# Performance work log

Measured on AMD Instinct MI355X. Metric: run time of the kernel, lower is better.

The kernel has to match this reference:

```python
import jax, jax.numpy as jnp
import numpy as np

IN_CH = 32
OUT_CH = 32
HIDDEN = 32  # edge/angle MLP hidden width


def setup_inputs() -> dict:
    key = jax.random.key(0)
    ks = jax.random.split(key, 13)
    N, E, A = 50000, 200000, 400000
    s = 0.1
    return {
        "x": jax.random.normal(ks[0], (N, IN_CH), dtype=jnp.float32),
        "edge_index": jax.random.randint(ks[1], (2, E), 0, N),
        "edge_attr": jax.random.uniform(ks[2], (E, 1), dtype=jnp.float32),
        "angle_index": jax.random.randint(ks[3], (3, A), 0, N),
        "angles": jax.random.uniform(ks[4], (A, 1), dtype=jnp.float32),
        # edge_mlp: Linear(1,32) -> ReLU -> Linear(32, in*out)
        "eW1": jax.random.normal(ks[5], (1, HIDDEN), dtype=jnp.float32) * s,
        "eb1": jax.random.normal(ks[6], (HIDDEN,), dtype=jnp.float32) * s,
        "eW2": jax.random.normal(ks[7], (HIDDEN, IN_CH * OUT_CH), dtype=jnp.float32) * s,
        "eb2": jax.random.normal(ks[8], (IN_CH * OUT_CH,), dtype=jnp.float32) * s,
        # angle_mlp: Linear(1,32) -> ReLU -> Linear(32, out)
        "aW1": jax.random.normal(ks[9], (1, HIDDEN), dtype=jnp.float32) * s,
        "ab1": jax.random.normal(ks[10], (HIDDEN,), dtype=jnp.float32) * s,
        "aW2": jax.random.normal(ks[11], (HIDDEN, OUT_CH), dtype=jnp.float32) * s,
        "ab2": jax.random.normal(ks[12], (OUT_CH,), dtype=jnp.float32) * s,
    }


def reference(x, edge_index, edge_attr, angle_index, angles,
              eW1, eb1, eW2, eb2, aW1, ab1, aW2, ab2):
    N = x.shape[0]
    row, col = edge_index[0], edge_index[1]
    # per-edge weight matrices from edge MLP: (E, in, out)
    h = jax.nn.relu(edge_attr @ eW1 + eb1)
    edge_w = (h @ eW2 + eb2).reshape(-1, IN_CH, OUT_CH)
    # gather source node features, apply per-edge matrix (bmm)
    msg = jnp.einsum('ei,eio->eo', x[col], edge_w)  # (E, out)
    agg = jax.ops.segment_sum(msg, row, num_segments=N)
    # angle branch: scatter angle features onto center node j
    j = angle_index[1]
    angle_feat = jax.nn.relu(angles @ aW1 + ab1) @ aW2 + ab2  # (A, out)
    agg = agg + jax.ops.segment_sum(angle_feat, j, num_segments=N)
    return agg
```

## Files before the change

kernel.cpp:

```cpp
#include <hip/hip_runtime.h>
#include <hip/hip_bf16.h>
#include <stdint.h>

#define IC 32
#define OC 32
#define HID 32

#define PBIN 16
#define TSH 44
#define TSCALE 1048576.0f

#define PBE 12
#define MAXN 65536

typedef __attribute__((ext_vector_type(8))) _Float16 half8;
typedef __attribute__((ext_vector_type(4))) float f32x4;
typedef unsigned long long u64;

static __device__ __forceinline__ _Float16 f2h(float f) { return (_Float16)f; }

__device__ __align__(16) _Float16 g_MK[PBE * 2 * 32 * 32];
__device__ float g_ekn[16];
__device__ float g_akn[16];
__device__ int   g_npc[2];
__device__ __align__(16) u64 g_cells[(size_t)MAXN * PBIN];

__global__ __launch_bounds__(512) void setup_zero(
    const float* __restrict__ eW1, const float* __restrict__ eb1,
    const float* __restrict__ eW2, const float* __restrict__ eb2,
    const float* __restrict__ aW1, const float* __restrict__ ab1,
    float* __restrict__ out, int outF4, int cellF4)
{
    __shared__ float ts_s[32];
    __shared__ int   rk_s[32];
    __shared__ int   re_s[32];
    const int tid = threadIdx.x;
    const int bid = blockIdx.x;

    if (bid < 48) {
        if (bid == 0 && tid < 16) { g_ekn[tid] = 1e30f; g_akn[tid] = 1e30f; }
        if (tid < 32) {
            const int k = tid;
            const float w = eW1[k], b = eb1[k];
            const float ts = -b / w;
            const bool re = (w != 0.f) && (ts > 0.f) && (ts < 1.f);
            int rk = 0;
            for (int k2 = 0; k2 < 32; ++k2) {
                const float w2 = eW1[k2], b2 = eb1[k2];
                const float t2 = -b2 / w2;
                const bool re2 = (w2 != 0.f) && (t2 > 0.f) && (t2 < 1.f);
                rk += (re2 && (t2 < ts || (t2 == ts && k2 < k))) ? 1 : 0;
            }
            ts_s[k] = ts; rk_s[k] = rk; re_s[k] = re ? 1 : 0;
        }
        __syncthreads();

        if (bid == 0) {
            if (tid < 32) {
                if (re_s[tid]) g_ekn[rk_s[tid]] = ts_s[tid];
                if (tid == 0) {
                    int n = 0;
                    for (int k = 0; k < 32; ++k) n += re_s[k];
                    g_npc[0] = n + 1;
                }
            } else if (tid < 64) {
                const int k = tid - 32;
                const float w = aW1[k], b = ab1[k];
                const float ts = -b / w;
                const bool re = (w != 0.f) && (ts > 0.f) && (ts < 1.f);
                int rk = 0, nre = 0;
                for (int k2 = 0; k2 < 32; ++k2) {
                    const float w2 = aW1[k2], b2 = ab1[k2];
                    const float t2 = -b2 / w2;
                    const bool re2 = (w2 != 0.f) && (t2 > 0.f) && (t2 < 1.f);
                    nre += re2 ? 1 : 0;
                    rk += (re2 && (t2 < ts || (t2 == ts && k2 < k))) ? 1 : 0;
                }
                if (re) g_akn[rk] = ts;
                if (k == 0) g_npc[1] = nre + 1;
            }
        }

        const int gid = bid * 512 + tid;
        if (gid < PBE * 2 * 32 * 32) {
            const int i   = gid & 31;
            const int o   = (gid >> 5) & 31;
            const int mat = (gid >> 10) & 1;
            const int cc  = gid >> 11;
            float acc = (mat == 0) ? eb2[i * 32 + o] : 0.f;
            for (int k = 0; k < 32; ++k) {
                const bool flip = re_s[k] && (rk_s[k] < cc);
                const float w = eW1[k], b = eb1[k];
                const bool on0 = b > 0.f;
                const bool on = (w > 0.f) ? (on0 || flip) : (on0 && !flip);
                if (on) acc = fmaf((mat == 0 ? b : w),
                                   eW2[k * 1024 + i * 32 + o], acc);
            }
            g_MK[((cc * 2 + mat) * 32 + o) * 32 + i] = (_Float16)acc;
        }
    }

    const int total = outF4 + cellF4;
    const float4 z4 = make_float4(0.f, 0.f, 0.f, 0.f);
    for (int i = bid * 512 + tid; i < total; i += gridDim.x * 512) {
        if (i < outF4) ((float4*)out)[i] = z4;
        else           ((float4*)g_cells)[i - outF4] = z4;
    }
}

__global__ __launch_bounds__(256) void angle_scatter(
    const float* __restrict__ angles, const int* __restrict__ angle_index,
    u64* __restrict__ cells, int A)
{
    u64* cp = cells ? cells : g_cells;
    float kn[16];
#pragma unroll
    for (int j = 0; j < 16; ++j) kn[j] = g_akn[j];

    int i0 = blockIdx.x * blockDim.x + threadIdx.x;
    int stride = gridDim.x * blockDim.x;
    for (int a = i0; a < A; a += stride) {
        const float t = angles[a];
        const int j = angle_index[A + a];
        int cc = 0;
#pragma unroll
        for (int jj = 0; jj < 16; ++jj) cc += (t >= kn[jj]) ? 1 : 0;
        if ((unsigned)cc < (unsigned)PBIN) {
            const u64 enc = ((u64)1 << TSH) | (u64)(unsigned)(t * TSCALE);
            atomicAdd(cp + (size_t)j * PBIN + cc, enc);
        }
    }
}

static __device__ __forceinline__ void angle_gather_wave(
    const u64* __restrict__ cells, float* __restrict__ out,
    const float* __restrict__ aW1, const float* __restrict__ ab1,
    const float* __restrict__ aW2, const float* __restrict__ ab2,
    int N, int base, int lane, bool addmode)
{
    const int q = lane >> 4, l15 = lane & 15;
    float w1s[8], b1s[8];
    int c0 = 0, c1 = 0;
#pragma unroll
    for (int k = 0; k < HID; ++k) {
        const float w = aW1[k], b = ab1[k];
        const bool pos = w > 0.f;
        const bool f0 = pos ? (b > 0.f) : !(b > 0.f);
        const bool f1 = pos ? ((w + b) > 0.f) : !((w + b) > 0.f);
        c0 += f0 ? 1 : 0;
        c1 += f1 ? 1 : 0;
        if ((k >> 3) == q) { w1s[k & 7] = w; b1s[k & 7] = b; }
    }
    int npc = c1 - c0 + 1;
    if (npc > PBIN) npc = PBIN;

    half8 Bf0, Bf1;
#pragma unroll
    for (int j = 0; j < 8; ++j) {
        Bf0[j] = f2h(aW2[(q * 8 + j) * OC + l15]);
        Bf1[j] = f2h(aW2[(q * 8 + j) * OC + 16 + l15]);
    }
    const float bias0 = ab2[l15];
    const float bias1 = ab2[16 + l15];

    const int jn = base + l15;
    const bool vn = (jn < N);
    const u64* cj = cells + (size_t)(vn ? jn : 0) * PBIN;
    float g[8] = {0.f, 0.f, 0.f, 0.f, 0.f, 0.f, 0.f, 0.f};
    float tot = 0.f;
    for (int cc = 0; cc < npc; ++cc) {
        const u64 v = vn ? cj[cc] : 0;
        if (v) {
            const float n  = (float)(unsigned)(v >> TSH);
            const float ts = (float)(v & (((u64)1 << TSH) - 1)) * (1.f / TSCALE);
            const float tb = ts / n;
#pragma unroll
            for (int k = 0; k < 8; ++k) {
                float h = fmaf(tb, w1s[k], b1s[k]);
                h = h > 0.f ? h : 0.f;
                g[k] = fmaf(n, h, g[k]);
            }
            tot += n;
        }
    }
    half8 a;
#pragma unroll
    for (int k = 0; k < 8; ++k) a[k] = f2h(g[k]);

    f32x4 acc0 = {0.f, 0.f, 0.f, 0.f};
    f32x4 acc1 = {0.f, 0.f, 0.f, 0.f};
    acc0 = __builtin_amdgcn_mfma_f32_16x16x32_f16(a, Bf0, acc0, 0, 0, 0);
    acc1 = __builtin_amdgcn_mfma_f32_16x16x32_f16(a, Bf1, acc1, 0, 0, 0);

#pragma unroll
    for (int r = 0; r < 4; ++r) {
        const int node = base + q * 4 + r;
        const float tr = __shfl(tot, q * 4 + r, 64);
        if (node < N) {
            const float v0 = fmaf(tr, bias0, acc0[r]);
            const float v1 = fmaf(tr, bias1, acc1[r]);
            if (addmode) {
                unsafeAtomicAdd(out + (size_t)node * OC + l15, v0);
                unsafeAtomicAdd(out + (size_t)node * OC + 16 + l15, v1);
            } else {
                out[(size_t)node * OC + l15]      = v0;
                out[(size_t)node * OC + 16 + l15] = v1;
            }
        }
    }
}

__global__ __launch_bounds__(256) void angle_gather_ow(
    float* __restrict__ out,
    const float* __restrict__ aW1, const float* __restrict__ ab1,
    const float* __restrict__ aW2, const float* __restrict__ ab2, int N)
{
    const int lane = threadIdx.x & 63;
    const int wib  = threadIdx.x >> 6;
    const int base = (blockIdx.x * 4 + wib) * 16;
    if (base >= N) return;
    angle_gather_wave((const u64*)out, out, aW1, ab1, aW2, ab2,
                      N, base, lane, false);
}

__global__ __launch_bounds__(512, 4) void mega_kernel(
    const float* __restrict__ x, const int* __restrict__ edge_index,
    const float* __restrict__ edge_attr,
    const float* __restrict__ eW1, const float* __restrict__ eb1,
    const float* __restrict__ eW2, const float* __restrict__ eb2,
    const float* __restrict__ angles, const int* __restrict__ angle_index,
    const float* __restrict__ aW1, const float* __restrict__ ab1,
    const float* __restrict__ aW2, const float* __restrict__ ab2,
    float* __restrict__ out, int E, int A, int N,
    int EB, int GB, int FA, int FE)
{
    __shared__ __align__(16) _Float16 B[PBE * 2 * 32 * 40];
    __shared__ float knl[16];

    const int tid = threadIdx.x;
    const int bid = blockIdx.x;

    if (bid < EB) {
        for (int r = tid; r < PBE * 2 * 32; r += 512) {
            const float4* s = (const float4*)(g_MK + r * 32);
            float4 a0 = s[0], a1 = s[1], a2 = s[2], a3 = s[3];
            float4* d = (float4*)(B + r * 40);
            d[0] = a0; d[1] = a1; d[2] = a2; d[3] = a3;
        }
        if (tid < 16) knl[tid] = g_ekn[tid];
        __syncthreads();

        float kn[PBE];
#pragma unroll
        for (int j = 0; j < PBE; ++j) kn[j] = knl[j];
        int npc = g_npc[0];
        if (npc > PBE) npc = PBE;

        const int lane  = tid & 63;
        const int w8    = tid >> 6;
        const int gwave = bid * 8 + w8;
        const int ot    = gwave & 1;
        const int tile0 = gwave >> 1;
        const int tstride = (EB * 8) >> 1;
        const int q     = lane >> 4;
        const int l15   = lane & 15;
        const int ocol  = ot * 16 + l15;
        const _Float16* Bbase = B + (size_t)ocol * 40 + q * 8;

        const int numTiles = (E + 15) >> 4;

        for (int tile = tile0; tile < numTiles; tile += 2 * tstride) {
            const int tA = tile;
            const int tB = tile + tstride;
            const bool hasB = (tB < numTiles);

            const int eA  = (tA << 4) + l15;
            const bool va = (eA < E);
            const float ta = va ? edge_attr[eA] : 0.f;
            const int colA = va ? edge_index[E + eA] : 0;

            const int eB  = (tB << 4) + l15;
            const bool vb = hasB && (eB < E);
            const float tb = vb ? edge_attr[eB] : 0.f;
            const int colB = vb ? edge_index[E + eB] : 0;

            const float* xpA = x + (size_t)colA * IC + q * 8;
            const float4 xloA = *(const float4*)(xpA);
            const float4 xhiA = *(const float4*)(xpA + 4);
            const float* xpB = x + (size_t)colB * IC + q * 8;
            const float4 xloB = *(const float4*)(xpB);
            const float4 xhiB = *(const float4*)(xpB + 4);

            int dstsA[4], dstsB[4];
            const int ebaseA = (tA << 4) + q * 4;
            const int ebaseB = (tB << 4) + q * 4;
#pragma unroll
            for (int r = 0; r < 4; ++r) {
                const int erA = ebaseA + r;
                dstsA[r] = (erA < E) ? edge_index[erA] : -1;
                const int erB = ebaseB + r;
                dstsB[r] = (hasB && erB < E) ? edge_index[erB] : -1;
            }

            int ccA = 0, ccB = 0;
#pragma unroll
            for (int j = 0; j < PBE; ++j) {
                ccA += (ta >= kn[j]) ? 1 : 0;
                ccB += (tb >= kn[j]) ? 1 : 0;
            }

            half8 xhA, xhB;
            xhA[0] = f2h(xloA.x); xhA[1] = f2h(xloA.y);
            xhA[2] = f2h(xloA.z); xhA[3] = f2h(xloA.w);
            xhA[4] = f2h(xhiA.x); xhA[5] = f2h(xhiA.y);
            xhA[6] = f2h(xhiA.z); xhA[7] = f2h(xhiA.w);
            xhB[0] = f2h(xloB.x); xhB[1] = f2h(xloB.y);
            xhB[2] = f2h(xloB.z); xhB[3] = f2h(xloB.w);
            xhB[4] = f2h(xhiB.x); xhB[5] = f2h(xhiB.y);
            xhB[6] = f2h(xhiB.z); xhB[7] = f2h(xhiB.w);

            const _Float16 thA = f2h(ta), thB = f2h(tb);
            const half8 tvA = {thA, thA, thA, thA, thA, thA, thA, thA};
            const half8 tvB = {thB, thB, thB, thB, thB, thB, thB, thB};
            const half8 xtA = xhA * tvA;
            const half8 xtB = xhB * tvB;
            const half8 z = {0, 0, 0, 0, 0, 0, 0, 0};

            f32x4 accA = {0.f, 0.f, 0.f, 0.f};
            f32x4 accB = {0.f, 0.f, 0.f, 0.f};
            for (int c = 0; c < npc; ++c) {
                const half8 bM = *(const half8*)(Bbase + (size_t)(c * 2 + 0) * 32 * 40);
                const half8 bK = *(const half8*)(Bbase + (size_t)(c * 2 + 1) * 32 * 40);
                const half8 aA1 = (ccA == c) ? xhA : z;
                const half8 aA2 = (ccA == c) ? xtA : z;
                const half8 aB1 = (ccB == c) ? xhB : z;
                const half8 aB2 = (ccB == c) ? xtB : z;
                accA = __builtin_amdgcn_mfma_f32_16x16x32_f16(aA1, bM, accA, 0, 0, 0);
                accB = __builtin_amdgcn_mfma_f32_16x16x32_f16(aB1, bM, accB, 0, 0, 0);
                accA = __builtin_amdgcn_mfma_f32_16x16x32_f16(aA2, bK, accA, 0, 0, 0);
                accB = __builtin_amdgcn_mfma_f32_16x16x32_f16(aB2, bK, accB, 0, 0, 0);
            }

#pragma unroll
            for (int r = 0; r < 4; ++r) {
                if (dstsA[r] >= 0)
                    unsafeAtomicAdd(out + (size_t)dstsA[r] * OC + ocol, accA[r]);
            }
#pragma unroll
            for (int r = 0; r < 4; ++r) {
                if (dstsB[r] >= 0)
                    unsafeAtomicAdd(out + (size_t)dstsB[r] * OC + ocol, accB[r]);
            }
        }
    } else if (bid < EB + GB) {
        const int lane = tid & 63;
        const int wib  = tid >> 6;
        const int base = ((bid - EB) * 8 + wib) * 16;
        if (base < N)
            angle_gather_wave(g_cells, out, aW1, ab1, aW2, ab2,
                              N, base, lane, true);
    } else if (bid < EB + GB + FA) {
        if (g_npc[1] <= PBIN) return;
        const float kn15 = g_akn[15];
        float w1[HID], b1[HID];
#pragma unroll
        for (int k = 0; k < HID; ++k) { w1[k] = aW1[k]; b1[k] = ab1[k]; }
        int i0 = (bid - EB - GB) * 512 + tid;
        int stride = FA * 512;
        for (int a = i0; a < A; a += stride) {
            const float t = angles[a];
            if (t < kn15) continue;
            const int j = angle_index[A + a];
            float h[HID];
#pragma unroll
            for (int k = 0; k < HID; ++k) {
                float v = fmaf(t, w1[k], b1[k]);
                h[k] = v > 0.f ? v : 0.f;
            }
            for (int o = 0; o < OC; ++o) {
                float s = ab2[o];
#pragma unroll
                for (int k = 0; k < HID; ++k) s = fmaf(h[k], aW2[k * OC + o], s);
                unsafeAtomicAdd(out + (size_t)j * OC + o, s);
            }
        }
    } else {
        if (g_npc[0] <= PBE) return;
        const float knb = g_ekn[PBE - 1];
        int i0 = (bid - EB - GB - FA) * 512 + tid;
        int stride = FE * 512;
        for (int e = i0; e < E; e += stride) {
            const float t = edge_attr[e];
            if (t < knb) continue;
            const int col = edge_index[E + e];
            const int dst = edge_index[e];
            float h[HID];
#pragma unroll
            for (int k = 0; k < HID; ++k) {
                float v = fmaf(t, eW1[k], eb1[k]);
                h[k] = v > 0.f ? v : 0.f;
            }
            for (int o = 0; o < OC; ++o) {
                float s = 0.f;
                for (int i = 0; i < IC; ++i) {
                    float wio = eb2[i * 32 + o];
#pragma unroll
                    for (int k = 0; k < HID; ++k)
                        wio = fmaf(h[k], eW2[k * 1024 + i * 32 + o], wio);
                    s = fmaf(x[(size_t)col * IC + i], wio, s);
                }
                unsafeAtomicAdd(out + (size_t)dst * OC + o, s);
            }
        }
    }
}

extern "C" void kernel_launch(void* const* d_in, const int* in_sizes, int n_in,
                              void* d_out, int out_size, void* d_ws, size_t ws_size,
                              hipStream_t stream)
{
    const float* x          = (const float*)d_in[0];
    const int*   edge_index = (const int*)d_in[1];
    const float* edge_attr  = (const float*)d_in[2];
    const int*   angle_index= (const int*)d_in[3];
    const float* angles     = (const float*)d_in[4];
    const float* eW1        = (const float*)d_in[5];
    const float* eb1        = (const float*)d_in[6];
    const float* eW2        = (const float*)d_in[7];
    const float* eb2        = (const float*)d_in[8];
    const float* aW1        = (const float*)d_in[9];
    const float* ab1        = (const float*)d_in[10];
    const float* aW2        = (const float*)d_in[11];
    const float* ab2        = (const float*)d_in[12];
    float* out = (float*)d_out;
    (void)d_ws; (void)ws_size;

    const int E = in_sizes[1] / 2;
    const int A = in_sizes[3] / 3;
    const int N = in_sizes[0] / IC;

    const int outF4 = out_size / 4;
    const int sblocks = (A + 255) / 256;

    if (N <= MAXN) {
        const int cellF4 = N * 8;
        int zg = (outF4 + cellF4 + 511) / 512;
        if (zg < 48) zg = 48;
        setup_zero<<<zg, 512, 0, stream>>>(eW1, eb1, eW2, eb2, aW1, ab1,
                                           out, outF4, cellF4);

        angle_scatter<<<sblocks, 256, 0, stream>>>(angles, angle_index,
                                                   nullptr, A);

        const int EB = 512;
        const int GB = (N + 127) / 128;
        const int FA = 64, FE = 64;
        mega_kernel<<<EB + GB + FA + FE, 512, 0, stream>>>(
            x, edge_index, edge_attr, eW1, eb1, eW2, eb2,
            angles, angle_index, aW1, ab1, aW2, ab2,
            out, E, A, N, EB, GB, FA, FE);
    } else {
        int zg = (outF4 + 511) / 512;
        if (zg < 48) zg = 48;
        setup_zero<<<zg, 512, 0, stream>>>(eW1, eb1, eW2, eb2, aW1, ab1,
                                           out, outF4, 0);
        angle_scatter<<<sblocks, 256, 0, stream>>>(angles, angle_index,
                                                   (u64*)out, A);
        angle_gather_ow<<<(N + 63) / 64, 256, 0, stream>>>(out, aW1, ab1,
                                                           aW2, ab2, N);
        const int EB = 512, FA = 64, FE = 64;
        mega_kernel<<<EB + FA + FE, 512, 0, stream>>>(
            x, edge_index, edge_attr, eW1, eb1, eW2, eb2,
            angles, angle_index, aW1, ab1, aW2, ab2,
            out, E, A, N, EB, 0, FA, FE);
    }
}
```

Measured before the change: 155.2 us.

## Bucket edges by destination node to reduce output atomics

While scattering angles, the kernel also builds fixed-size per-destination buckets of up to 8 edges, each stored as a packed (attr, col) entry. Edges beyond 8 per node go to an overflow list, which a new block group processes on the scalar path. The MFMA edge tiles now cover two nodes of 8 slots each, sum their rows in registers and issue one atomic per node and output column instead of one per edge. The goal is fewer global float atomics, paid for by a counter-atomic build pass and MFMA work wasted on empty bucket slots.

```diff
diff --git a/kernel.cpp b/kernel.cpp
--- a/kernel.cpp
+++ b/kernel.cpp
@@ -12,6 +12,8 @@
 
 #define PBE 12
 #define MAXN 65536
+#define MAXE (1 << 20)
+#define BKTD 8
 
 typedef __attribute__((ext_vector_type(8))) _Float16 half8;
 typedef __attribute__((ext_vector_type(4))) float f32x4;
@@ -24,18 +26,24 @@
 __device__ float g_akn[16];
 __device__ int   g_npc[2];
 __device__ __align__(16) u64 g_cells[(size_t)MAXN * PBIN];
+__device__ __align__(16) u64 g_bkt[(size_t)MAXN * BKTD];
+__device__ __align__(16) unsigned g_cnt[MAXN];
+__device__ __align__(16) unsigned g_ovf[MAXE];
+__device__ unsigned g_ovfn;
 
 __global__ __launch_bounds__(512) void setup_zero(
     const float* __restrict__ eW1, const float* __restrict__ eb1,
     const float* __restrict__ eW2, const float* __restrict__ eb2,
     const float* __restrict__ aW1, const float* __restrict__ ab1,
-    float* __restrict__ out, int outF4, int cellF4)
+    float* __restrict__ out, int outF4, int cellF4, int cntF4)
 {
     __shared__ float ts_s[32];
     __shared__ int   rk_s[32];
     __shared__ int   re_s[32];
     const int tid = threadIdx.x;
     const int bid = blockIdx.x;
+
+    if (bid == 0 && tid == 0) g_ovfn = 0u;
 
     if (bid < 48) {
         if (bid == 0 && tid < 16) { g_ekn[tid] = 1e30f; g_akn[tid] = 1e30f; }
@@ -100,25 +108,28 @@
         }
     }
 
-    const int total = outF4 + cellF4;
+    const int total = outF4 + cellF4 + cntF4;
     const float4 z4 = make_float4(0.f, 0.f, 0.f, 0.f);
     for (int i = bid * 512 + tid; i < total; i += gridDim.x * 512) {
-        if (i < outF4) ((float4*)out)[i] = z4;
-        else           ((float4*)g_cells)[i - outF4] = z4;
+        if (i < outF4)               ((float4*)out)[i] = z4;
+        else if (i < outF4 + cellF4) ((float4*)g_cells)[i - outF4] = z4;
+        else                         ((float4*)g_cnt)[i - outF4 - cellF4] = z4;
     }
 }
 
 __global__ __launch_bounds__(256) void angle_scatter(
     const float* __restrict__ angles, const int* __restrict__ angle_index,
-    u64* __restrict__ cells, int A)
+    const float* __restrict__ edge_attr, const int* __restrict__ edge_index,
+    u64* __restrict__ cells, int A, int E, int doBuild)
 {
     u64* cp = cells ? cells : g_cells;
     float kn[16];
 #pragma unroll
     for (int j = 0; j < 16; ++j) kn[j] = g_akn[j];
 
-    int i0 = blockIdx.x * blockDim.x + threadIdx.x;
-    int stride = gridDim.x * blockDim.x;
+    const int i0 = blockIdx.x * blockDim.x + threadIdx.x;
+    const int stride = gridDim.x * blockDim.x;
+
     for (int a = i0; a < A; a += stride) {
         const float t = angles[a];
         const int j = angle_index[A + a];
@@ -128,6 +139,22 @@
         if ((unsigned)cc < (unsigned)PBIN) {
             const u64 enc = ((u64)1 << TSH) | (u64)(unsigned)(t * TSCALE);
             atomicAdd(cp + (size_t)j * PBIN + cc, enc);
+        }
+    }
+
+    if (doBuild) {
+        for (int e = i0; e < E; e += stride) {
+            const float t  = edge_attr[e];
+            const int dst  = edge_index[e];
+            const int col  = edge_index[E + e];
+            const unsigned pos = atomicAdd(&g_cnt[dst], 1u);
+            if (pos < BKTD) {
+                g_bkt[(size_t)dst * BKTD + pos] =
+                    ((u64)__float_as_uint(t) << 32) | (unsigned)col;
+            } else {
+                const unsigned oi = atomicAdd(&g_ovfn, 1u);
+                if (oi < MAXE) g_ovf[oi] = (unsigned)e;
+            }
         }
     }
 }
@@ -232,7 +259,7 @@
     const float* __restrict__ aW1, const float* __restrict__ ab1,
     const float* __restrict__ aW2, const float* __restrict__ ab2,
     float* __restrict__ out, int E, int A, int N,
-    int EB, int GB, int FA, int FE)
+    int EB, int GB, int FA, int FE, int useBkt)
 {
     __shared__ __align__(16) _Float16 B[PBE * 2 * 32 * 40];
     __shared__ float knl[16];
@@ -265,91 +292,177 @@
         const int q     = lane >> 4;
         const int l15   = lane & 15;
         const int ocol  = ot * 16 + l15;
-        const _Float16* Bbase = B + (size_t)ocol * 40 + q * 8;
-
-        const int numTiles = (E + 15) >> 4;
-
-        for (int tile = tile0; tile < numTiles; tile += 2 * tstride) {
-            const int tA = tile;
-            const int tB = tile + tstride;
-            const bool hasB = (tB < numTiles);
-
-            const int eA  = (tA << 4) + l15;
-            const bool va = (eA < E);
-            const float ta = va ? edge_attr[eA] : 0.f;
-            const int colA = va ? edge_index[E + eA] : 0;
-
-            const int eB  = (tB << 4) + l15;
-            const bool vb = hasB && (eB < E);
-            const float tb = vb ? edge_attr[eB] : 0.f;
-            const int colB = vb ? edge_index[E + eB] : 0;
-
-            const float* xpA = x + (size_t)colA * IC + q * 8;
-            const float4 xloA = *(const float4*)(xpA);
-            const float4 xhiA = *(const float4*)(xpA + 4);
-            const float* xpB = x + (size_t)colB * IC + q * 8;
-            const float4 xloB = *(const float4*)(xpB);
-            const float4 xhiB = *(const float4*)(xpB + 4);
-
-            int dstsA[4], dstsB[4];
-            const int ebaseA = (tA << 4) + q * 4;
-            const int ebaseB = (tB << 4) + q * 4;
-#pragma unroll
-            for (int r = 0; r < 4; ++r) {
-                const int erA = ebaseA + r;
-                dstsA[r] = (erA < E) ? edge_index[erA] : -1;
-                const int erB = ebaseB + r;
-                dstsB[r] = (hasB && erB < E) ? edge_index[erB] : -1;
-            }
-
-            int ccA = 0, ccB = 0;
-#pragma unroll
-            for (int j = 0; j < PBE; ++j) {
-                ccA += (ta >= kn[j]) ? 1 : 0;
-                ccB += (tb >= kn[j]) ? 1 : 0;
-            }
-
-            half8 xhA, xhB;
-            xhA[0] = f2h(xloA.x); xhA[1] = f2h(xloA.y);
-            xhA[2] = f2h(xloA.z); xhA[3] = f2h(xloA.w);
-            xhA[4] = f2h(xhiA.x); xhA[5] = f2h(xhiA.y);
-            xhA[6] = f2h(xhiA.z); xhA[7] = f2h(xhiA.w);
-            xhB[0] = f2h(xloB.x); xhB[1] = f2h(xloB.y);
-            xhB[2] = f2h(xloB.z); xhB[3] = f2h(xloB.w);
-            xhB[4] = f2h(xhiB.x); xhB[5] = f2h(xhiB.y);
-            xhB[6] = f2h(xhiB.z); xhB[7] = f2h(xhiB.w);
-
-            const _Float16 thA = f2h(ta), thB = f2h(tb);
-            const half8 tvA = {thA, thA, thA, thA, thA, thA, thA, thA};
-            const half8 tvB = {thB, thB, thB, thB, thB, thB, thB, thB};
-            const half8 xtA = xhA * tvA;
-            const half8 xtB = xhB * tvB;
-            const half8 z = {0, 0, 0, 0, 0, 0, 0, 0};
-
-            f32x4 accA = {0.f, 0.f, 0.f, 0.f};
-            f32x4 accB = {0.f, 0.f, 0.f, 0.f};
-            for (int c = 0; c < npc; ++c) {
-                const half8 bM = *(const half8*)(Bbase + (size_t)(c * 2 + 0) * 32 * 40);
-                const half8 bK = *(const half8*)(Bbase + (size_t)(c * 2 + 1) * 32 * 40);
-                const half8 aA1 = (ccA == c) ? xhA : z;
-                const half8 aA2 = (ccA == c) ? xtA : z;
-                const half8 aB1 = (ccB == c) ? xhB : z;
-                const half8 aB2 = (ccB == c) ? xtB : z;
-                accA = __builtin_amdgcn_mfma_f32_16x16x32_f16(aA1, bM, accA, 0, 0, 0);
-                accB = __builtin_amdgcn_mfma_f32_16x16x32_f16(aB1, bM, accB, 0, 0, 0);
-                accA = __builtin_amdgcn_mfma_f32_16x16x32_f16(aA2, bK, accA, 0, 0, 0);
-                accB = __builtin_amdgcn_mfma_f32_16x16x32_f16(aB2, bK, accB, 0, 0, 0);
-            }
-
-#pragma unroll
-            for (int r = 0; r < 4; ++r) {
-                if (dstsA[r] >= 0)
-                    unsafeAtomicAdd(out + (size_t)dstsA[r] * OC + ocol, accA[r]);
-            }
-#pragma unroll
-            for (int r = 0; r < 4; ++r) {
-                if (dstsB[r] >= 0)
-                    unsafeAtomicAdd(out + (size_t)dstsB[r] * OC + ocol, accB[r]);
+        const _Float16* Bb = B + (size_t)ocol * 40 + q * 8;
+        const half8 z = {0, 0, 0, 0, 0, 0, 0, 0};
+
+        if (useBkt) {
+            const int numST = (N + 1) >> 1;
+            for (int tile = tile0; tile < numST; tile += 2 * tstride) {
+                const int tA = tile;
+                const int tB = tile + tstride;
+                const bool hasB = (tB < numST);
+
+                const int slotA = (tA << 4) + l15;
+                const int nodeA = slotA >> 3;
+                const unsigned cAn = (nodeA < N) ? g_cnt[nodeA] : 0u;
+                const bool va = (unsigned)(l15 & 7) < (cAn < BKTD ? cAn : BKTD);
+                const u64 pkA = va ? g_bkt[slotA] : 0ull;
+                const float ta = __uint_as_float((unsigned)(pkA >> 32));
+                const int colA = (int)(unsigned)(pkA & 0xffffffffu);
+
+                const int slotB = (tB << 4) + l15;
+                const int nodeB = slotB >> 3;
+                const unsigned cBn = (hasB && nodeB < N) ? g_cnt[nodeB] : 0u;
+                const bool vb = (unsigned)(l15 & 7) < (cBn < BKTD ? cBn : BKTD);
+                const u64 pkB = vb ? g_bkt[slotB] : 0ull;
+                const float tb = __uint_as_float((unsigned)(pkB >> 32));
+                const int colB = (int)(unsigned)(pkB & 0xffffffffu);
+
+                const float* xpA = x + (size_t)colA * IC + q * 8;
+                const float4 xloA = *(const float4*)(xpA);
+                const float4 xhiA = *(const float4*)(xpA + 4);
+                const float* xpB = x + (size_t)colB * IC + q * 8;
+                const float4 xloB = *(const float4*)(xpB);
+                const float4 xhiB = *(const float4*)(xpB + 4);
+
+                int ccA = 0, ccB = 0;
+#pragma unroll
+                for (int j = 0; j < PBE; ++j) {
+                    ccA += (ta >= kn[j]) ? 1 : 0;
+                    ccB += (tb >= kn[j]) ? 1 : 0;
+                }
+                if (!va) ccA = -1;
+                if (!vb) ccB = -1;
+
+                half8 xhA, xhB;
+                xhA[0] = f2h(xloA.x); xhA[1] = f2h(xloA.y);
+                xhA[2] = f2h(xloA.z); xhA[3] = f2h(xloA.w);
+                xhA[4] = f2h(xhiA.x); xhA[5] = f2h(xhiA.y);
+                xhA[6] = f2h(xhiA.z); xhA[7] = f2h(xhiA.w);
+                xhB[0] = f2h(xloB.x); xhB[1] = f2h(xloB.y);
+                xhB[2] = f2h(xloB.z); xhB[3] = f2h(xloB.w);
+                xhB[4] = f2h(xhiB.x); xhB[5] = f2h(xhiB.y);
+                xhB[6] = f2h(xhiB.z); xhB[7] = f2h(xhiB.w);
+
+                const _Float16 thA = f2h(ta), thB = f2h(tb);
+                const half8 tvA = {thA, thA, thA, thA, thA, thA, thA, thA};
+                const half8 tvB = {thB, thB, thB, thB, thB, thB, thB, thB};
+                const half8 xtA = xhA * tvA;
+                const half8 xtB = xhB * tvB;
+
+                f32x4 accA = {0.f, 0.f, 0.f, 0.f};
+                f32x4 accB = {0.f, 0.f, 0.f, 0.f};
+                for (int c = 0; c < npc; ++c) {
+                    const half8 bM = *(const half8*)(Bb + (size_t)(c * 2 + 0) * 32 * 40);
+                    const half8 bK = *(const half8*)(Bb + (size_t)(c * 2 + 1) * 32 * 40);
+                    const half8 aA1 = (ccA == c) ? xhA : z;
+                    const half8 aA2 = (ccA == c) ? xtA : z;
+                    const half8 aB1 = (ccB == c) ? xhB : z;
+                    const half8 aB2 = (ccB == c) ? xtB : z;
+                    accA = __builtin_amdgcn_mfma_f32_16x16x32_f16(aA1, bM, accA, 0, 0, 0);
+                    accB = __builtin_amdgcn_mfma_f32_16x16x32_f16(aB1, bM, accB, 0, 0, 0);
+                    accA = __builtin_amdgcn_mfma_f32_16x16x32_f16(aA2, bK, accA, 0, 0, 0);
+                    accB = __builtin_amdgcn_mfma_f32_16x16x32_f16(aB2, bK, accB, 0, 0, 0);
+                }
+
+                float sA = accA[0] + accA[1] + accA[2] + accA[3];
+                float sB = accB[0] + accB[1] + accB[2] + accB[3];
+                sA += __shfl_xor(sA, 16, 64);
+                sB += __shfl_xor(sB, 16, 64);
+                if (!(q & 1)) {
+                    const int nA = (tA << 1) + (q >> 1);
+                    if (nA < N && g_cnt[nA] > 0u)
+                        unsafeAtomicAdd(out + (size_t)nA * OC + ocol, sA);
+                    if (hasB) {
+                        const int nB = (tB << 1) + (q >> 1);
+                        if (nB < N && g_cnt[nB] > 0u)
+                            unsafeAtomicAdd(out + (size_t)nB * OC + ocol, sB);
+                    }
+                }
+            }
+        } else {
+            const int numTiles = (E + 15) >> 4;
+            for (int tile = tile0; tile < numTiles; tile += 2 * tstride) {
+                const int tA = tile;
+                const int tB = tile + tstride;
+                const bool hasB = (tB < numTiles);
+
+                const int eA  = (tA << 4) + l15;
+                const bool va = (eA < E);
+                const float ta = va ? edge_attr[eA] : 0.f;
+                const int colA = va ? edge_index[E + eA] : 0;
+
+                const int eB  = (tB << 4) + l15;
+                const bool vb = hasB && (eB < E);
+                const float tb = vb ? edge_attr[eB] : 0.f;
+                const int colB = vb ? edge_index[E + eB] : 0;
+
+                const float* xpA = x + (size_t)colA * IC + q * 8;
+                const float4 xloA = *(const float4*)(xpA);
+                const float4 xhiA = *(const float4*)(xpA + 4);
+                const float* xpB = x + (size_t)colB * IC + q * 8;
+                const float4 xloB = *(const float4*)(xpB);
+                const float4 xhiB = *(const float4*)(xpB + 4);
+
+                int dstsA[4], dstsB[4];
+                const int ebaseA = (tA << 4) + q * 4;
+                const int ebaseB = (tB << 4) + q * 4;
+#pragma unroll
+                for (int r = 0; r < 4; ++r) {
+                    const int erA = ebaseA + r;
+                    dstsA[r] = (erA < E) ? edge_index[erA] : -1;
+                    const int erB = ebaseB + r;
+                    dstsB[r] = (hasB && erB < E) ? edge_index[erB] : -1;
+                }
+
+                int ccA = 0, ccB = 0;
+#pragma unroll
+                for (int j = 0; j < PBE; ++j) {
+                    ccA += (ta >= kn[j]) ? 1 : 0;
+                    ccB += (tb >= kn[j]) ? 1 : 0;
+                }
+
+                half8 xhA, xhB;
+                xhA[0] = f2h(xloA.x); xhA[1] = f2h(xloA.y);
+                xhA[2] = f2h(xloA.z); xhA[3] = f2h(xloA.w);
+                xhA[4] = f2h(xhiA.x); xhA[5] = f2h(xhiA.y);
+                xhA[6] = f2h(xhiA.z); xhA[7] = f2h(xhiA.w);
+                xhB[0] = f2h(xloB.x); xhB[1] = f2h(xloB.y);
+                xhB[2] = f2h(xloB.z); xhB[3] = f2h(xloB.w);
+                xhB[4] = f2h(xhiB.x); xhB[5] = f2h(xhiB.y);
+                xhB[6] = f2h(xhiB.z); xhB[7] = f2h(xhiB.w);
+
+                const _Float16 thA = f2h(ta), thB = f2h(tb);
+                const half8 tvA = {thA, thA, thA, thA, thA, thA, thA, thA};
+                const half8 tvB = {thB, thB, thB, thB, thB, thB, thB, thB};
+                const half8 xtA = xhA * tvA;
+                const half8 xtB = xhB * tvB;
+
+                f32x4 accA = {0.f, 0.f, 0.f, 0.f};
+                f32x4 accB = {0.f, 0.f, 0.f, 0.f};
+                for (int c = 0; c < npc; ++c) {
+                    const half8 bM = *(const half8*)(Bb + (size_t)(c * 2 + 0) * 32 * 40);
+                    const half8 bK = *(const half8*)(Bb + (size_t)(c * 2 + 1) * 32 * 40);
+                    const half8 aA1 = (ccA == c) ? xhA : z;
+                    const half8 aA2 = (ccA == c) ? xtA : z;
+                    const half8 aB1 = (ccB == c) ? xhB : z;
+                    const half8 aB2 = (ccB == c) ? xtB : z;
+                    accA = __builtin_amdgcn_mfma_f32_16x16x32_f16(aA1, bM, accA, 0, 0, 0);
+                    accB = __builtin_amdgcn_mfma_f32_16x16x32_f16(aB1, bM, accB, 0, 0, 0);
+                    accA = __builtin_amdgcn_mfma_f32_16x16x32_f16(aA2, bK, accA, 0, 0, 0);
+                    accB = __builtin_amdgcn_mfma_f32_16x16x32_f16(aB2, bK, accB, 0, 0, 0);
+                }
+
+#pragma unroll
+                for (int r = 0; r < 4; ++r) {
+                    if (dstsA[r] >= 0)
+                        unsafeAtomicAdd(out + (size_t)dstsA[r] * OC + ocol, accA[r]);
+                }
+#pragma unroll
+                for (int r = 0; r < 4; ++r) {
+                    if (dstsB[r] >= 0)
+                        unsafeAtomicAdd(out + (size_t)dstsB[r] * OC + ocol, accB[r]);
+                }
             }
         }
     } else if (bid < EB + GB) {
@@ -384,7 +497,7 @@
                 unsafeAtomicAdd(out + (size_t)j * OC + o, s);
             }
         }
-    } else {
+    } else if (bid < EB + GB + FA + FE) {
         if (g_npc[0] <= PBE) return;
         const float knb = g_ekn[PBE - 1];
         int i0 = (bid - EB - GB - FA) * 512 + tid;
@@ -409,6 +522,37 @@
                         wio = fmaf(h[k], eW2[k * 1024 + i * 32 + o], wio);
                     s = fmaf(x[(size_t)col * IC + i], wio, s);
                 }
+                unsafeAtomicAdd(out + (size_t)dst * OC + o, s);
+            }
+        }
+    } else {
+        unsigned nov = g_ovfn;
+        if (nov > MAXE) nov = MAXE;
+        float kn[PBE];
+#pragma unroll
+        for (int j = 0; j < PBE; ++j) kn[j] = g_ekn[j];
+        const int OVB = 32;
+        int i0 = (bid - EB - GB - FA - FE) * 512 + tid;
+        int stride = OVB * 512;
+        for (unsigned i = (unsigned)i0; i < nov; i += stride) {
+            const int e = (int)g_ovf[i];
+            const float t = edge_attr[e];
+            int cc = 0;
+#pragma unroll
+            for (int j = 0; j < PBE; ++j) cc += (t >= kn[j]) ? 1 : 0;
+            if (cc >= PBE) continue;
+            const int col = edge_index[E + e];
+            const int dst = edge_index[e];
+            float xv[IC];
+#pragma unroll
+            for (int i2 = 0; i2 < IC; ++i2) xv[i2] = x[(size_t)col * IC + i2];
+            for (int o = 0; o < OC; ++o) {
+                const _Float16* mr = g_MK + ((size_t)(cc * 2 + 0) * 32 + o) * 32;
+                const _Float16* kr = g_MK + ((size_t)(cc * 2 + 1) * 32 + o) * 32;
+                float s = 0.f;
+#pragma unroll
+                for (int i2 = 0; i2 < IC; ++i2)
+                    s = fmaf(fmaf(t, (float)kr[i2], (float)mr[i2]), xv[i2], s);
                 unsafeAtomicAdd(out + (size_t)dst * OC + o, s);
             }
         }
@@ -441,37 +585,41 @@
 
     const int outF4 = out_size / 4;
     const int sblocks = (A + 255) / 256;
-
-    if (N <= MAXN) {
+    const bool fast = (N <= MAXN) && (E <= MAXE);
+
+    if (fast) {
         const int cellF4 = N * 8;
-        int zg = (outF4 + cellF4 + 511) / 512;
+        const int cntF4  = (N + 3) / 4;
+        int zg = (outF4 + cellF4 + cntF4 + 511) / 512;
         if (zg < 48) zg = 48;
         setup_zero<<<zg, 512, 0, stream>>>(eW1, eb1, eW2, eb2, aW1, ab1,
-                                           out, outF4, cellF4);
+                                           out, outF4, cellF4, cntF4);
 
         angle_scatter<<<sblocks, 256, 0, stream>>>(angles, angle_index,
-                                                   nullptr, A);
+                                                   edge_attr, edge_index,
+                                                   nullptr, A, E, 1);
 
         const int EB = 512;
         const int GB = (N + 127) / 128;
-        const int FA = 64, FE = 64;
-        mega_kernel<<<EB + GB + FA + FE, 512, 0, stream>>>(
+        const int FA = 64, FE = 64, OV = 32;
+        mega_kernel<<<EB + GB + FA + FE + OV, 512, 0, stream>>>(
             x, edge_index, edge_attr, eW1, eb1, eW2, eb2,
             angles, angle_index, aW1, ab1, aW2, ab2,
-            out, E, A, N, EB, GB, FA, FE);
+            out, E, A, N, EB, GB, FA, FE, 1);
     } else {
         int zg = (outF4 + 511) / 512;
         if (zg < 48) zg = 48;
         setup_zero<<<zg, 512, 0, stream>>>(eW1, eb1, eW2, eb2, aW1, ab1,
-                                           out, outF4, 0);
+                                           out, outF4, 0, 0);
         angle_scatter<<<sblocks, 256, 0, stream>>>(angles, angle_index,
-                                                   (u64*)out, A);
+                                                   edge_attr, edge_index,
+                                                   (u64*)out, A, E, 0);
         angle_gather_ow<<<(N + 63) / 64, 256, 0, stream>>>(out, aW1, ab1,
                                                            aW2, ab2, N);
         const int EB = 512, FA = 64, FE = 64;
         mega_kernel<<<EB + FA + FE, 512, 0, stream>>>(
             x, edge_index, edge_attr, eW1, eb1, eW2, eb2,
             angles, angle_index, aW1, ab1, aW2, ab2,
-            out, E, A, N, EB, 0, FA, FE);
+            out, E, A, N, EB, 0, FA, FE, 0);
     }
 }
```

Measured after the change: 227.2 us. +46.3%, slower.
